# Optimization experiments

Measured on AMD Instinct MI355X. Metric: run time of the kernel, lower is better.

## Reference

```python
import jax, jax.numpy as jnp
import numpy as np

B, L, D = 32768, 256, 16  # batch, chain length, bond dim; physical dim d=2


def setup_inputs() -> dict:
    key = jax.random.key(0)
    k_phi, k_first, k_mid, k_last = jax.random.split(key, 4)
    scale = 1.0 / np.sqrt(2.0 * D)  # variance-preserving chain
    phi_batch = jax.random.normal(k_phi, (B, L, 2), dtype=jnp.float32)
    core_first = jax.random.normal(k_first, (2, D), dtype=jnp.float32) * scale
    cores_mid = jax.random.normal(k_mid, (L - 2, D, 2, D), dtype=jnp.float32) * scale
    core_last = jax.random.normal(k_last, (D, 2), dtype=jnp.float32) * scale
    out_bias = jnp.zeros((), dtype=jnp.float32)
    return {
        "phi_batch": phi_batch,
        "core_first": core_first,
        "cores_mid": cores_mid,
        "core_last": core_last,
        "out_bias": out_bias,
    }


def reference(phi_batch, core_first, cores_mid, core_last, out_bias):
    # MPS / tensor-train contraction, batched over samples.
    # Each sample contracts feature vectors phi[i] (len-2) into the physical
    # index of core i, then chains the resulting D x D matrices via a
    # left-to-right bond-space matvec (what cotengra would find per-sample).
    # v0: [B, D] = phi[:,0] contracted with first core [2, D]
    v0 = jnp.einsum("bp,pd->bd", phi_batch[:, 0], core_first)

    # middle features, scan-major layout: [L-2, B, 2]
    phis_mid = jnp.swapaxes(phi_batch[:, 1:-1], 0, 1)

    def step(v, xs):
        phi_t, core = xs  # phi_t: [B, 2], core: [D, 2, D]
        # contract bond then physical index; never materialize [B, D, D]
        u = jnp.einsum("bq,qpr->bpr", v, core)   # [B, 2, D]
        v_new = jnp.einsum("bp,bpr->br", phi_t, u)  # [B, D]
        return v_new, None

    v, _ = jax.lax.scan(step, v0, (phis_mid, cores_mid))

    # close the chain with last core [D, 2] and last feature [B, 2]
    out = jnp.einsum("bq,qp,bp->b", v, core_last, phi_batch[:, -1])
    return out + out_bias
```

## Files before the change

### kernel.cpp

```cpp
#include <hip/hip_runtime.h>
#include <stdint.h>


typedef short  bf16x8 __attribute__((ext_vector_type(8)));
typedef float  f32x4  __attribute__((ext_vector_type(4)));
typedef int    i32x4  __attribute__((ext_vector_type(4)));
typedef unsigned int u32;

#define NSLOT 128
#define BWD_OFF (NSLOT*2*64)
#define NCHUNK 32

#define PACK_HI(hi, lo) ((int)__builtin_amdgcn_perm((u32)(hi), (u32)(lo), 0x07060302u))

__device__ __forceinline__ u32 rne_bump(u32 u){
  return u + 0x7FFFu + ((u >> 16) & 1u);
}

__device__ __forceinline__ void async16(const void* g, void* l){
  __builtin_amdgcn_global_load_lds(
    (const __attribute__((address_space(1))) u32*)(uintptr_t)g,
    (__attribute__((address_space(3))) u32*)(uintptr_t)l, 16, 0, 0);
}

__global__ void build_frags(const float* __restrict__ cm, i32x4* __restrict__ ws)
{
  const int bid  = blockIdx.x;
  const int p    = threadIdx.x >> 6;
  const int lane = threadIdx.x & 63;
  const int m    = lane & 15;
  const int g    = lane >> 4;
  const bool fwd = bid < NSLOT;
  const int slot = fwd ? bid : (bid - NSLOT);
  const int t    = fwd ? bid : (253 - slot);
  i32x4* dst = ws + (fwd ? 0 : BWD_OFF) + (slot*2 + p)*64 + lane;
  i32x4 w;
  #pragma unroll
  for(int d=0; d<4; ++d){
    u32 h[2];
    #pragma unroll
    for(int e=0; e<2; ++e){
      const int j = 2*d + e;
      const int q = 4*g + (j & 3);
      const bool hi_part = (j < 4);
      const int ci = fwd ? ((((t*16 + q)*2) + p)*16 + m)
                         : ((((t*16 + m)*2) + p)*16 + q);
      const float c = cm[ci];
      const u32 u  = __float_as_uint(c);
      const u32 a  = rne_bump(u);
      const float hif = __uint_as_float(a & 0xFFFF0000u);
      const u32 b  = rne_bump(__float_as_uint(c - hif));
      h[e] = hi_part ? (a >> 16) : (b >> 16);
    }
    w[d] = (int)(h[0] | (h[1] << 16));
  }
  *dst = w;
}

__global__ __launch_bounds__(256, 4) void mps_chain(
  const float* __restrict__ phi,
  const float* __restrict__ core_first,
  const float* __restrict__ core_last,
  const float* __restrict__ bias,
  const i32x4* __restrict__ ws,
  float* __restrict__ out)
{
  const int lane = threadIdx.x & 63;
  const int wv   = threadIdx.x >> 6;
  const int b0   = blockIdx.x * 32;
  const int n    = lane & 15;
  const int g    = lane >> 4;
  const int half = wv & 1;
  const int s_in = half*16 + n;
  const bool isFwd = (wv < 2);

  __shared__ i32x4 fragF[2][4][2][64];
  __shared__ i32x4 fragB[2][4][2][64];
  __shared__ float2 phF[2][2][64][2];
  __shared__ float2 phB[2][2][64][2];

  const float* phiRow = phi + (size_t)(b0 + s_in) * 512;

  const float* phiDmaBase = phi + (size_t)(b0 + half*16 + (lane >> 2)) * 512
                                + (lane & 3) * 4;
  const i32x4* wsD = isFwd ? ws : (ws + BWD_OFF);

  auto issue_dma = [&](int c, int buf){
    #pragma unroll
    for (int jj = 0; jj < 2; ++jj){
      const int j = half*2 + jj;
      const int slot = c*4 + j;
      #pragma unroll
      for (int p = 0; p < 2; ++p){
        const i32x4* gp = wsD + (slot*2 + p)*64 + lane;
        void* lp = isFwd ? (void*)&fragF[buf][j][p][0]
                         : (void*)&fragB[buf][j][p][0];
        async16(gp, lp);
      }
    }
    const int w = isFwd ? 4*c : (248 - 4*c);
    const float* gp = phiDmaBase + 2*w;
    void* lp = isFwd ? (void*)&phF[buf][half][0][0]
                     : (void*)&phB[buf][half][0][0];
    async16(gp, lp);
  };

  float v[4];
  i32x4 bfr;

  auto make_bfrag = [&](){
    const u32 u0 = __float_as_uint(v[0]), u1 = __float_as_uint(v[1]);
    const u32 u2 = __float_as_uint(v[2]), u3 = __float_as_uint(v[3]);
    const float l0 = v[0] - __uint_as_float(u0 & 0xFFFF0000u);
    const float l1 = v[1] - __uint_as_float(u1 & 0xFFFF0000u);
    const float l2 = v[2] - __uint_as_float(u2 & 0xFFFF0000u);
    const float l3 = v[3] - __uint_as_float(u3 & 0xFFFF0000u);
    bfr[0] = PACK_HI(u1, u0);
    bfr[1] = PACK_HI(u3, u2);
    bfr[2] = PACK_HI(__float_as_uint(l1), __float_as_uint(l0));
    bfr[3] = PACK_HI(__float_as_uint(l3), __float_as_uint(l2));
  };

  auto step = [&](const i32x4& a0, const i32x4& a1, float phx, float phy){
    i32x4 sw; sw[0]=bfr[2]; sw[1]=bfr[3]; sw[2]=bfr[0]; sw[3]=bfr[1];
    const bf16x8 bh = __builtin_bit_cast(bf16x8, bfr);
    const bf16x8 bs = __builtin_bit_cast(bf16x8, sw);
    f32x4 acc0 = {0.f,0.f,0.f,0.f};
    f32x4 acc1 = {0.f,0.f,0.f,0.f};
    acc0 = __builtin_amdgcn_mfma_f32_16x16x32_bf16(__builtin_bit_cast(bf16x8, a0), bh, acc0, 0,0,0);
    acc0 = __builtin_amdgcn_mfma_f32_16x16x32_bf16(__builtin_bit_cast(bf16x8, a0), bs, acc0, 0,0,0);
    acc1 = __builtin_amdgcn_mfma_f32_16x16x32_bf16(__builtin_bit_cast(bf16x8, a1), bh, acc1, 0,0,0);
    acc1 = __builtin_amdgcn_mfma_f32_16x16x32_bf16(__builtin_bit_cast(bf16x8, a1), bs, acc1, 0,0,0);
    v[0] = phx*acc0[0] + phy*acc1[0];
    v[1] = phx*acc0[1] + phy*acc1[1];
    v[2] = phx*acc0[2] + phy*acc1[2];
    v[3] = phx*acc0[3] + phy*acc1[3];
    make_bfrag();
  };

  if (isFwd){
    const float2 ph0 = *(const float2*)phiRow;
    #pragma unroll
    for(int reg=0; reg<4; ++reg){
      const int r = g*4 + reg;
      v[reg] = ph0.x * core_first[r] + ph0.y * core_first[16 + r];
    }
  } else {
    const float4 fL = *(const float4*)(phiRow + 508);
    #pragma unroll
    for(int reg=0; reg<4; ++reg){
      const int r = g*4 + reg;
      v[reg] = fL.z * core_last[2*r] + fL.w * core_last[2*r + 1];
    }
  }
  make_bfrag();

  issue_dma(0, 0);
  __syncthreads();

  const int limit = isFwd ? 128 : 126;
  const i32x4 (*fragD)[4][2][64] = isFwd ? fragF : fragB;
  const float2 (*phD)[2][64][2]  = isFwd ? phF : phB;

  #pragma unroll 1
  for (int c = 0; c < NCHUNK; ++c){
    const int buf = c & 1;
    if (c + 1 < NCHUNK) issue_dma(c + 1, buf ^ 1);
    #pragma unroll
    for (int i = 0; i < 4; ++i){
      if (c*4 + i < limit){
        const int o = isFwd ? (1 + i) : (6 - i);
        const float2 ph = phD[buf][half][n*4 + (o >> 1)][o & 1];
        const i32x4 a0 = fragD[buf][i][0][lane];
        const i32x4 a1 = fragD[buf][i][1][lane];
        step(a0, a1, ph.x, ph.y);
      }
    }
    __syncthreads();
  }

  float* red = (float*)&fragF[0][0][0][0];
  *(float4*)&red[((isFwd ? 0 : 1)*32 + s_in)*20 + 4*g] =
      make_float4(v[0], v[1], v[2], v[3]);
  __syncthreads();
  if (threadIdx.x < 32){
    const int s = threadIdx.x;
    float acc = bias[0];
    #pragma unroll
    for(int q = 0; q < 16; ++q)
      acc += red[s*20 + q] * red[(32 + s)*20 + q];
    out[b0 + s] = acc;
  }
}

extern "C" void kernel_launch(void* const* d_in, const int* in_sizes, int n_in,
                              void* d_out, int out_size, void* d_ws, size_t ws_size,
                              hipStream_t stream)
{
  const float* phi  = (const float*)d_in[0];
  const float* cf   = (const float*)d_in[1];
  const float* cm   = (const float*)d_in[2];
  const float* cl   = (const float*)d_in[3];
  const float* bias = (const float*)d_in[4];
  i32x4* ws = (i32x4*)d_ws;

  build_frags<<<256, 128, 0, stream>>>(cm, ws);
  mps_chain<<<1024, 256, 0, stream>>>(phi, cf, cl, bias, ws, (float*)d_out);
}
```

Measured before the change: 142.6 us.

## Precontract adjacent core pairs to halve serial chain steps

A preprocessing kernel now multiplies each pair of adjacent middle cores into four 16x16 matrices (one per pair of physical indices), stored as split-bf16 MFMA fragments. The chain kernel then advances two sites per step: it weights the four products by the outer product of the two feature vectors. This halves the length of the serial dependency chain per sample, at the cost of twice the MFMAs per step and extra error from rounding the pair products. The LDS and DMA layout changes to match the pair structure, and the backward direction handles an odd leftover pair.

```diff
diff --git a/kernel.cpp b/kernel.cpp
--- a/kernel.cpp
+++ b/kernel.cpp
@@ -7,15 +7,14 @@
 typedef int    i32x4  __attribute__((ext_vector_type(4)));
 typedef unsigned int u32;
 
-#define NSLOT 128
-#define BWD_OFF (NSLOT*2*64)
+#define NPF 64
+#define NPB 63
+#define BWD_OFF (NPF*4*64)
 #define NCHUNK 32
 
 #define PACK_HI(hi, lo) ((int)__builtin_amdgcn_perm((u32)(hi), (u32)(lo), 0x07060302u))
 
-__device__ __forceinline__ u32 rne_bump(u32 u){
-  return u + 0x7FFFu + ((u >> 16) & 1u);
-}
+__device__ __forceinline__ u32 rne_bump(u32 u){ return u + 0x7FFFu + ((u >> 16) & 1u); }
 
 __device__ __forceinline__ void async16(const void* g, void* l){
   __builtin_amdgcn_global_load_lds(
@@ -23,38 +22,48 @@
     (__attribute__((address_space(3))) u32*)(uintptr_t)l, 16, 0, 0);
 }
 
-__global__ void build_frags(const float* __restrict__ cm, i32x4* __restrict__ ws)
+__global__ void build_pair_frags(const float* __restrict__ cm, i32x4* __restrict__ ws)
 {
-  const int bid  = blockIdx.x;
-  const int p    = threadIdx.x >> 6;
+  __shared__ float Ca[512], Cb[512];
+  const int bid = blockIdx.x;
+  const bool fwd = bid < NPF;
+  const int j  = fwd ? bid : bid - NPF;
+  const int ta = fwd ? 2*j     : 252 - 2*j;
+  const int tb = fwd ? 2*j + 1 : 253 - 2*j;
+  {
+    const float* A = cm + ta*512;
+    const float* B = cm + tb*512;
+    for (int i = threadIdx.x; i < 512; i += 256){ Ca[i] = A[i]; Cb[i] = B[i]; }
+  }
+  __syncthreads();
+  const int f    = threadIdx.x >> 6;
   const int lane = threadIdx.x & 63;
   const int m    = lane & 15;
   const int g    = lane >> 4;
-  const bool fwd = bid < NSLOT;
-  const int slot = fwd ? bid : (bid - NSLOT);
-  const int t    = fwd ? bid : (253 - slot);
-  i32x4* dst = ws + (fwd ? 0 : BWD_OFF) + (slot*2 + p)*64 + lane;
+  const int p    = f >> 1, q = f & 1;
+  u32 hi[4], lo[4];
+  #pragma unroll
+  for (int x = 0; x < 4; ++x){
+    const int cq = 4*g + x;
+    float acc = 0.f;
+    #pragma unroll
+    for (int r = 0; r < 16; ++r){
+      const float a = fwd ? Ca[cq*32 + p*16 + r] : Ca[m*32 + p*16 + r];
+      const float b = fwd ? Cb[r*32 + q*16 + m]  : Cb[r*32 + q*16 + cq];
+      acc = fmaf(a, b, acc);
+    }
+    const u32 u  = __float_as_uint(acc);
+    const u32 aa = rne_bump(u);
+    const float hf = __uint_as_float(aa & 0xFFFF0000u);
+    const u32 bb = rne_bump(__float_as_uint(acc - hf));
+    hi[x] = aa >> 16; lo[x] = bb >> 16;
+  }
   i32x4 w;
-  #pragma unroll
-  for(int d=0; d<4; ++d){
-    u32 h[2];
-    #pragma unroll
-    for(int e=0; e<2; ++e){
-      const int j = 2*d + e;
-      const int q = 4*g + (j & 3);
-      const bool hi_part = (j < 4);
-      const int ci = fwd ? ((((t*16 + q)*2) + p)*16 + m)
-                         : ((((t*16 + m)*2) + p)*16 + q);
-      const float c = cm[ci];
-      const u32 u  = __float_as_uint(c);
-      const u32 a  = rne_bump(u);
-      const float hif = __uint_as_float(a & 0xFFFF0000u);
-      const u32 b  = rne_bump(__float_as_uint(c - hif));
-      h[e] = hi_part ? (a >> 16) : (b >> 16);
-    }
-    w[d] = (int)(h[0] | (h[1] << 16));
-  }
-  *dst = w;
+  w[0] = (int)(hi[0] | (hi[1] << 16));
+  w[1] = (int)(hi[2] | (hi[3] << 16));
+  w[2] = (int)(lo[0] | (lo[1] << 16));
+  w[3] = (int)(lo[2] | (lo[3] << 16));
+  ws[(fwd ? 0 : BWD_OFF) + (j*4 + f)*64 + lane] = w;
 }
 
 __global__ __launch_bounds__(256, 4) void mps_chain(
@@ -73,36 +82,26 @@
   const int half = wv & 1;
   const int s_in = half*16 + n;
   const bool isFwd = (wv < 2);
-
-  __shared__ i32x4 fragF[2][4][2][64];
-  __shared__ i32x4 fragB[2][4][2][64];
-  __shared__ float2 phF[2][2][64][2];
-  __shared__ float2 phB[2][2][64][2];
+  const int dirIdx = isFwd ? 0 : 1;
+
+  __shared__ i32x4 frag[2][2][2][4][64];
+  __shared__ float phL[2][2][2][4][16][4];
 
   const float* phiRow = phi + (size_t)(b0 + s_in) * 512;
 
-  const float* phiDmaBase = phi + (size_t)(b0 + half*16 + (lane >> 2)) * 512
-                                + (lane & 3) * 4;
+  const float* phiDma = phi + (size_t)(b0 + 16*half + (lane & 15)) * 512
+                            + (lane >> 4) * 4;
   const i32x4* wsD = isFwd ? ws : (ws + BWD_OFF);
 
-  auto issue_dma = [&](int c, int buf){
-    #pragma unroll
-    for (int jj = 0; jj < 2; ++jj){
-      const int j = half*2 + jj;
-      const int slot = c*4 + j;
-      #pragma unroll
-      for (int p = 0; p < 2; ++p){
-        const i32x4* gp = wsD + (slot*2 + p)*64 + lane;
-        void* lp = isFwd ? (void*)&fragF[buf][j][p][0]
-                         : (void*)&fragB[buf][j][p][0];
-        async16(gp, lp);
-      }
-    }
-    const int w = isFwd ? 4*c : (248 - 4*c);
-    const float* gp = phiDmaBase + 2*w;
-    void* lp = isFwd ? (void*)&phF[buf][half][0][0]
-                     : (void*)&phB[buf][half][0][0];
-    async16(gp, lp);
+  auto issue_dma = [&](int cn, int buf){
+    int pr = 2*cn + half;
+    if (!isFwd && pr > NPB-1) pr = NPB-1;
+    const i32x4* base = wsD + pr*4*64 + lane;
+    #pragma unroll
+    for (int f = 0; f < 4; ++f)
+      async16(base + f*64, &frag[dirIdx][buf][half][f][0]);
+    const int W = isFwd ? 4*cn : (248 - 4*cn);
+    async16(phiDma + 2*W, &phL[dirIdx][buf][half][0][0][0]);
   };
 
   float v[4];
@@ -121,74 +120,86 @@
     bfr[3] = PACK_HI(__float_as_uint(l3), __float_as_uint(l2));
   };
 
-  auto step = [&](const i32x4& a0, const i32x4& a1, float phx, float phy){
+  auto pair_step = [&](const i32x4& G0, const i32x4& G1, const i32x4& G2,
+                       const i32x4& G3, float2 cA, float2 cB){
+    const float c00 = cA.x*cB.x, c01 = cA.x*cB.y;
+    const float c10 = cA.y*cB.x, c11 = cA.y*cB.y;
     i32x4 sw; sw[0]=bfr[2]; sw[1]=bfr[3]; sw[2]=bfr[0]; sw[3]=bfr[1];
     const bf16x8 bh = __builtin_bit_cast(bf16x8, bfr);
     const bf16x8 bs = __builtin_bit_cast(bf16x8, sw);
-    f32x4 acc0 = {0.f,0.f,0.f,0.f};
-    f32x4 acc1 = {0.f,0.f,0.f,0.f};
-    acc0 = __builtin_amdgcn_mfma_f32_16x16x32_bf16(__builtin_bit_cast(bf16x8, a0), bh, acc0, 0,0,0);
-    acc0 = __builtin_amdgcn_mfma_f32_16x16x32_bf16(__builtin_bit_cast(bf16x8, a0), bs, acc0, 0,0,0);
-    acc1 = __builtin_amdgcn_mfma_f32_16x16x32_bf16(__builtin_bit_cast(bf16x8, a1), bh, acc1, 0,0,0);
-    acc1 = __builtin_amdgcn_mfma_f32_16x16x32_bf16(__builtin_bit_cast(bf16x8, a1), bs, acc1, 0,0,0);
-    v[0] = phx*acc0[0] + phy*acc1[0];
-    v[1] = phx*acc0[1] + phy*acc1[1];
-    v[2] = phx*acc0[2] + phy*acc1[2];
-    v[3] = phx*acc0[3] + phy*acc1[3];
+    const f32x4 z = {0.f,0.f,0.f,0.f};
+    f32x4 a00 = __builtin_amdgcn_mfma_f32_16x16x32_bf16(__builtin_bit_cast(bf16x8,G0), bh, z, 0,0,0);
+    a00 = __builtin_amdgcn_mfma_f32_16x16x32_bf16(__builtin_bit_cast(bf16x8,G0), bs, a00, 0,0,0);
+    f32x4 a01 = __builtin_amdgcn_mfma_f32_16x16x32_bf16(__builtin_bit_cast(bf16x8,G1), bh, z, 0,0,0);
+    a01 = __builtin_amdgcn_mfma_f32_16x16x32_bf16(__builtin_bit_cast(bf16x8,G1), bs, a01, 0,0,0);
+    f32x4 a10 = __builtin_amdgcn_mfma_f32_16x16x32_bf16(__builtin_bit_cast(bf16x8,G2), bh, z, 0,0,0);
+    a10 = __builtin_amdgcn_mfma_f32_16x16x32_bf16(__builtin_bit_cast(bf16x8,G2), bs, a10, 0,0,0);
+    f32x4 a11 = __builtin_amdgcn_mfma_f32_16x16x32_bf16(__builtin_bit_cast(bf16x8,G3), bh, z, 0,0,0);
+    a11 = __builtin_amdgcn_mfma_f32_16x16x32_bf16(__builtin_bit_cast(bf16x8,G3), bs, a11, 0,0,0);
+    #pragma unroll
+    for (int i2 = 0; i2 < 4; ++i2)
+      v[i2] = c00*a00[i2] + c01*a01[i2] + c10*a10[i2] + c11*a11[i2];
     make_bfrag();
   };
 
   if (isFwd){
     const float2 ph0 = *(const float2*)phiRow;
     #pragma unroll
-    for(int reg=0; reg<4; ++reg){
+    for (int reg = 0; reg < 4; ++reg){
       const int r = g*4 + reg;
       v[reg] = ph0.x * core_first[r] + ph0.y * core_first[16 + r];
     }
   } else {
-    const float4 fL = *(const float4*)(phiRow + 508);
-    #pragma unroll
-    for(int reg=0; reg<4; ++reg){
+    const float2 phL2 = *(const float2*)(phiRow + 510);
+    #pragma unroll
+    for (int reg = 0; reg < 4; ++reg){
       const int r = g*4 + reg;
-      v[reg] = fL.z * core_last[2*r] + fL.w * core_last[2*r + 1];
+      v[reg] = phL2.x * core_last[2*r] + phL2.y * core_last[2*r + 1];
     }
   }
   make_bfrag();
 
   issue_dma(0, 0);
   __syncthreads();
-
-  const int limit = isFwd ? 128 : 126;
-  const i32x4 (*fragD)[4][2][64] = isFwd ? fragF : fragB;
-  const float2 (*phD)[2][64][2]  = isFwd ? phF : phB;
 
   #pragma unroll 1
   for (int c = 0; c < NCHUNK; ++c){
     const int buf = c & 1;
     if (c + 1 < NCHUNK) issue_dma(c + 1, buf ^ 1);
-    #pragma unroll
-    for (int i = 0; i < 4; ++i){
-      if (c*4 + i < limit){
-        const int o = isFwd ? (1 + i) : (6 - i);
-        const float2 ph = phD[buf][half][n*4 + (o >> 1)][o & 1];
-        const i32x4 a0 = fragD[buf][i][0][lane];
-        const i32x4 a1 = fragD[buf][i][1][lane];
-        step(a0, a1, ph.x, ph.y);
-      }
+
+    const float* pb = &phL[dirIdx][buf][half][0][n][0];
+    const float2 xA0 = *(const float2*)(pb + (isFwd ?   2 : 130));
+    const float2 xB0 = *(const float2*)(pb + (isFwd ?  64 : 192));
+    const float2 xA1 = *(const float2*)(pb + 66);
+    const float2 xB1 = *(const float2*)(pb + 128);
+
+    {
+      const i32x4 G0 = frag[dirIdx][buf][0][0][lane];
+      const i32x4 G1 = frag[dirIdx][buf][0][1][lane];
+      const i32x4 G2 = frag[dirIdx][buf][0][2][lane];
+      const i32x4 G3 = frag[dirIdx][buf][0][3][lane];
+      pair_step(G0, G1, G2, G3, xA0, xB0);
+    }
+    if (isFwd || (2*c + 1) < NPB){
+      const i32x4 G0 = frag[dirIdx][buf][1][0][lane];
+      const i32x4 G1 = frag[dirIdx][buf][1][1][lane];
+      const i32x4 G2 = frag[dirIdx][buf][1][2][lane];
+      const i32x4 G3 = frag[dirIdx][buf][1][3][lane];
+      pair_step(G0, G1, G2, G3, xA1, xB1);
     }
     __syncthreads();
   }
 
-  float* red = (float*)&fragF[0][0][0][0];
-  *(float4*)&red[((isFwd ? 0 : 1)*32 + s_in)*20 + 4*g] =
+  float* red = (float*)&frag[0][0][0][0][0];
+  *(float4*)&red[(dirIdx*32 + s_in)*20 + 4*g] =
       make_float4(v[0], v[1], v[2], v[3]);
   __syncthreads();
   if (threadIdx.x < 32){
     const int s = threadIdx.x;
     float acc = bias[0];
     #pragma unroll
-    for(int q = 0; q < 16; ++q)
-      acc += red[s*20 + q] * red[(32 + s)*20 + q];
+    for (int qq = 0; qq < 16; ++qq)
+      acc += red[s*20 + qq] * red[(32 + s)*20 + qq];
     out[b0 + s] = acc;
   }
 }
@@ -204,6 +215,6 @@
   const float* bias = (const float*)d_in[4];
   i32x4* ws = (i32x4*)d_ws;
 
-  build_frags<<<256, 128, 0, stream>>>(cm, ws);
+  build_pair_frags<<<NPF + NPB, 256, 0, stream>>>(cm, ws);
   mps_chain<<<1024, 256, 0, stream>>>(phi, cf, cl, bias, ws, (float*)d_out);
 }
```

Result: faster. 138.0 us (-3.2%).
